# Kernel optimization log

Hardware: AMD Instinct MI355X
Metric: run time of the kernel (lower is better)

## Reference

```python
import jax, jax.numpy as jnp
import numpy as np

NUM_POINTS = 4_000_000
RADIUS = 2.5
IMG = 1024


def setup_inputs() -> dict:
    key = jax.random.key(0)
    k1, k2, k3, k4 = jax.random.split(key, 4)
    # Uniform sampling inside a sphere, mirroring the torch __init__
    phi = jax.random.uniform(k1, (NUM_POINTS,)) * 2 * np.pi
    costheta = jax.random.uniform(k2, (NUM_POINTS,)) * 2 - 1
    u = jax.random.uniform(k3, (NUM_POINTS,))
    theta = jnp.arccos(costheta)
    r = RADIUS * u ** (1.0 / 3.0)
    x = r * jnp.sin(theta) * jnp.cos(phi)
    y = r * jnp.sin(theta) * jnp.sin(phi)
    z = r * jnp.cos(theta)
    positions = jnp.stack([x, y, z], axis=-1).astype(jnp.float32)  # [N,3]
    colors = jax.random.uniform(k4, (NUM_POINTS, 3), dtype=jnp.float32)
    # Camera at origin looking down +z, points translated to z in [2.5, 7.5]
    camera_pose = jnp.eye(4, dtype=jnp.float32).at[2, 3].set(5.0)
    intrinsics = jnp.array([[800.0, 0.0, 512.0],
                            [0.0, 800.0, 512.0],
                            [0.0, 0.0, 1.0]], dtype=jnp.float32)
    return {"positions": positions, "colors": colors,
            "camera_pose": camera_pose, "intrinsics": intrinsics,
            "H": IMG, "W": IMG}


def reference(positions, colors, camera_pose, intrinsics, H, W):
    # points_cam = (R @ P^T)^T + t^T
    R = camera_pose[:3, :3]
    t = camera_pose[:3, 3]
    pc = positions @ R.T + t  # [N,3]
    x, y, z = pc[:, 0], pc[:, 1], pc[:, 2]
    fx, fy = intrinsics[0, 0], intrinsics[1, 1]
    cx, cy = intrinsics[0, 2], intrinsics[1, 2]
    u = fx * x / z + cx
    v = fy * y / z + cy
    # int() truncation toward zero, matching the torch loop
    xi = u.astype(jnp.int32)
    yi = v.astype(jnp.int32)
    valid = (xi >= 0) & (xi < W) & (yi >= 0) & (yi < H)
    n = positions.shape[0]
    pix = jnp.where(valid, yi * W + xi, H * W)  # invalid -> sentinel segment
    winner = jax.ops.segment_max(jnp.arange(n, dtype=jnp.int32), pix,
                                 num_segments=H * W + 1)[: H * W]
    has = winner >= 0  # empty segments get iinfo(int32).min
    img_flat = jnp.where(has[:, None],
                         colors[jnp.clip(winner, 0, n - 1)],
                         jnp.float32(0.0))  # [H*W, 3]
    img = img_flat.reshape(H, W, 3).transpose(2, 0, 1)[None]  # [1,3,H,W]
    return jnp.clip(img, 0.0, 1.0)
```

## Files before the change

kernel.cpp:

```cpp
#include <hip/hip_runtime.h>


#define NB      1024
#define TB      512
#define NT      1024
#define PPB_MAX 4096
#define IMGW    1024
#define IMGHW   (1024 * 1024)

__host__ __device__ __forceinline__ unsigned align8u(unsigned x) {
    return (x + 7u) & ~7u;
}

__global__ void __launch_bounds__(TB)
binsort_kernel(const float* __restrict__ pos,
               const float* __restrict__ pose,
               const float* __restrict__ intr,
               unsigned* __restrict__ bins,
               unsigned* __restrict__ histG,
               int n, int ppb, int region) {
    __shared__ unsigned stash[PPB_MAX];
    __shared__ unsigned h[NT];
    __shared__ unsigned base_[NT];
    __shared__ unsigned cur[NT];
    __shared__ unsigned sc[TB];

    int tid = threadIdx.x;
    for (int t = tid; t < NT; t += TB) h[t] = 0;
    __syncthreads();

    float r00 = pose[0], r01 = pose[1], r02 = pose[2],  t0 = pose[3];
    float r10 = pose[4], r11 = pose[5], r12 = pose[6],  t1 = pose[7];
    float r20 = pose[8], r21 = pose[9], r22 = pose[10], t2 = pose[11];
    float fx = intr[0], cx = intr[2];
    float fy = intr[4], cy = intr[5];

    int start = blockIdx.x * ppb;
    int cnt = min(start + ppb, n) - start;
    if (cnt < 0) cnt = 0;

    const float4* p4 = (const float4*)(pos + (size_t)3 * (size_t)start);
    for (int j4 = tid * 4; j4 < cnt; j4 += TB * 4) {
        int g = j4 >> 2;
        float4 A = p4[3 * g + 0];
        float4 B = p4[3 * g + 1];
        float4 C = p4[3 * g + 2];
        float xs0 = A.x, ys0 = A.y, zs0 = A.z;
        float xs1 = A.w, ys1 = B.x, zs1 = B.y;
        float xs2 = B.z, ys2 = B.w, zs2 = C.x;
        float xs3 = C.y, ys3 = C.z, zs3 = C.w;

        unsigned pv[4];
        #define PROJ(K, PX, PY, PZ)                                          \
        {                                                                    \
            float x = r00 * PX + r01 * PY + r02 * PZ + t0;                   \
            float y = r10 * PX + r11 * PY + r12 * PZ + t1;                   \
            float z = r20 * PX + r21 * PY + r22 * PZ + t2;                   \
            float u = fx * x / z + cx;                                       \
            float v = fy * y / z + cy;                                       \
            int xi = (int)u;                                                 \
            int yi = (int)v;                                                 \
            unsigned p = 0xFFFFFFFFu;                                        \
            if ((j4 + K) < cnt && xi >= 0 && xi < IMGW && yi >= 0 &&         \
                yi < IMGW) {                                                 \
                p = ((unsigned)yi << 10) | (unsigned)xi;                     \
                int tt = ((yi >> 5) << 5) + (xi >> 5);                       \
                atomicAdd(&h[tt], 1u);                                       \
            }                                                                \
            pv[K] = p;                                                       \
        }
        PROJ(0, xs0, ys0, zs0)
        PROJ(1, xs1, ys1, zs1)
        PROJ(2, xs2, ys2, zs2)
        PROJ(3, xs3, ys3, zs3)
        #undef PROJ

        if (j4 + 3 < cnt) {
            *(uint4*)&stash[j4] = make_uint4(pv[0], pv[1], pv[2], pv[3]);
        } else {
            for (int k = 0; k < 4 && j4 + k < cnt; ++k) stash[j4 + k] = pv[k];
        }
    }
    __syncthreads();

    unsigned c0 = h[2 * tid];
    unsigned c1 = h[2 * tid + 1];
    unsigned v = c0 + c1;
    sc[tid] = v;
    __syncthreads();
    for (int off = 1; off < TB; off <<= 1) {
        unsigned add = (tid >= off) ? sc[tid - off] : 0u;
        __syncthreads();
        v += add;
        sc[tid] = v;
        __syncthreads();
    }
    base_[2 * tid]     = v - c0 - c1;
    base_[2 * tid + 1] = v - c1;
    __syncthreads();

    for (int t = tid; t < NT; t += TB) {
        cur[t] = base_[t];
        histG[(size_t)t * NB + blockIdx.x] = (base_[t] << 16) | h[t];
    }
    __syncthreads();

    unsigned* myRegion = bins + (size_t)blockIdx.x * (size_t)region;
    for (int j = tid; j < cnt; j += TB) {
        unsigned pv = stash[j];
        if (pv == 0xFFFFFFFFu) continue;
        unsigned xi = pv & 1023u, yi = pv >> 10;
        unsigned t  = ((yi >> 5) << 5) + (xi >> 5);
        unsigned lp = ((yi & 31u) << 5) + (xi & 31u);
        unsigned slot = atomicAdd(&cur[t], 1u);
        myRegion[slot] = (lp << 22) | (unsigned)(start + j);
    }
}

__global__ void __launch_bounds__(TB)
paint_kernel(const unsigned* __restrict__ bins,
             const unsigned* __restrict__ histG,
             const float* __restrict__ colors,
             float* __restrict__ out,
             int region) {
    __shared__ unsigned win[NT];
    int t = blockIdx.x;
    int tid = threadIdx.x;
    for (int l = tid; l < NT; l += TB) win[l] = 0;
    __syncthreads();

    for (int b = tid; b < NB; b += TB) {
        unsigned pk = histG[(size_t)t * NB + b];
        unsigned sbase = pk >> 16, cnt = pk & 0xFFFFu;
        const unsigned* seg = bins + (size_t)b * (size_t)region + sbase;
        for (unsigned k = 0; k < cnt; ++k) {
            unsigned e = seg[k];
            atomicMax(&win[e >> 22], (e & 0x3FFFFFu) + 1u);
        }
    }
    __syncthreads();

    int tx = (t & 31) << 5, ty = (t >> 5) << 5;
    for (int l = tid; l < NT; l += TB) {
        unsigned w = win[l];
        float r = 0.0f, g = 0.0f, bl = 0.0f;
        if (w) {
            unsigned wi = w - 1u;
            r  = fminf(fmaxf(colors[3 * wi + 0], 0.0f), 1.0f);
            g  = fminf(fmaxf(colors[3 * wi + 1], 0.0f), 1.0f);
            bl = fminf(fmaxf(colors[3 * wi + 2], 0.0f), 1.0f);
        }
        int x = tx + (l & 31), y = ty + (l >> 5);
        int p = y * IMGW + x;
        out[p] = r;
        out[IMGHW + p] = g;
        out[2 * IMGHW + p] = bl;
    }
}


__global__ void proj_simple(const float* __restrict__ pos,
                            const float* __restrict__ pose,
                            const float* __restrict__ intr,
                            const int* __restrict__ Hp,
                            const int* __restrict__ Wp,
                            int* __restrict__ winner, int n) {
    int i = blockIdx.x * blockDim.x + threadIdx.x;
    if (i >= n) return;
    float px = pos[3 * i], py = pos[3 * i + 1], pz = pos[3 * i + 2];
    float x = pose[0] * px + pose[1] * py + pose[2]  * pz + pose[3];
    float y = pose[4] * px + pose[5] * py + pose[6]  * pz + pose[7];
    float z = pose[8] * px + pose[9] * py + pose[10] * pz + pose[11];
    float u = intr[0] * x / z + intr[2];
    float v = intr[4] * y / z + intr[5];
    int xi = (int)u, yi = (int)v;
    int W = *Wp, H = *Hp;
    if (xi >= 0 && xi < W && yi >= 0 && yi < H) atomicMax(&winner[yi * W + xi], i);
}

__global__ void paint_simple(const int* __restrict__ winner,
                             const float* __restrict__ colors,
                             float* __restrict__ out, int HW) {
    int p = blockIdx.x * blockDim.x + threadIdx.x;
    if (p >= HW) return;
    int w = winner[p];
    float r = 0.0f, g = 0.0f, b = 0.0f;
    if (w >= 0) {
        r = fminf(fmaxf(colors[3 * w + 0], 0.0f), 1.0f);
        g = fminf(fmaxf(colors[3 * w + 1], 0.0f), 1.0f);
        b = fminf(fmaxf(colors[3 * w + 2], 0.0f), 1.0f);
    }
    out[p] = r; out[HW + p] = g; out[2 * HW + p] = b;
}

extern "C" void kernel_launch(void* const* d_in, const int* in_sizes, int n_in,
                              void* d_out, int out_size, void* d_ws, size_t ws_size,
                              hipStream_t stream) {
    const float* positions = (const float*)d_in[0];
    const float* colors    = (const float*)d_in[1];
    const float* pose      = (const float*)d_in[2];
    const float* intr      = (const float*)d_in[3];
    const int*   Hp        = (const int*)d_in[4];
    const int*   Wp        = (const int*)d_in[5];
    float* out = (float*)d_out;

    int n  = in_sizes[0] / 3;
    int HW = out_size / 3;

    int ppb = ((n + NB - 1) / NB + 3) & ~3;
    int region = (int)align8u((unsigned)ppb);
    unsigned* bins  = (unsigned*)d_ws;
    unsigned* histG = bins + (size_t)NB * (size_t)region;
    size_t needFast = ((size_t)NB * region + (size_t)NT * NB) * sizeof(unsigned);

    bool fast = (HW == IMGHW) && (n >= 4096) && (ppb <= PPB_MAX) &&
                (n <= 4000000) && (ws_size >= needFast);

    if (fast) {
        binsort_kernel<<<NB, TB, 0, stream>>>(positions, pose, intr,
                                              bins, histG, n, ppb, region);
        paint_kernel<<<NT, TB, 0, stream>>>(bins, histG, colors, out, region);
        return;
    }

    int* winner = (int*)d_ws;
    const int block = 256;
    hipMemsetAsync(winner, 0xFF, (size_t)HW * sizeof(int), stream);
    int grid = (n + block - 1) / block;
    proj_simple<<<grid, block, 0, stream>>>(positions, pose, intr, Hp, Wp,
                                            winner, n);
    int grid2 = (HW + block - 1) / block;
    paint_simple<<<grid2, block, 0, stream>>>(winner, colors, out, HW);
}
```

Measured before the change: 70.71 us.

## Halve sort blocks, use 1024-thread binsort, align bin segments to 8

Cuts the binsort grid from 1024 to 512 blocks of 1024 threads, so each block handles about twice as many points and each thread owns one tile's histogram entry. Each tile's bin segment is now padded up to a multiple of 8 entries, with the per-block region enlarged to make room. The paint kernel assigns exactly one source block per thread, so each paint block walks half as many segments, each about twice as long. The aim is to reduce the number of histogram segments paint has to scan and to align segment starts. The cost is a larger shared stash, fewer resident binsort blocks, and longer serial per-thread loops in paint.

```diff
diff --git a/kernel.cpp b/kernel.cpp
--- a/kernel.cpp
+++ b/kernel.cpp
@@ -1,10 +1,11 @@
 #include <hip/hip_runtime.h>
 
 
-#define NB      1024
-#define TB      512
+#define NB      512
+#define TBS     1024
+#define TBP     512
 #define NT      1024
-#define PPB_MAX 4096
+#define PPB_MAX 7936
 #define IMGW    1024
 #define IMGHW   (1024 * 1024)
 
@@ -12,7 +13,7 @@
     return (x + 7u) & ~7u;
 }
 
-__global__ void __launch_bounds__(TB)
+__global__ void __launch_bounds__(TBS)
 binsort_kernel(const float* __restrict__ pos,
                const float* __restrict__ pose,
                const float* __restrict__ intr,
@@ -23,10 +24,10 @@
     __shared__ unsigned h[NT];
     __shared__ unsigned base_[NT];
     __shared__ unsigned cur[NT];
-    __shared__ unsigned sc[TB];
+    __shared__ unsigned sc[TBS];
 
     int tid = threadIdx.x;
-    for (int t = tid; t < NT; t += TB) h[t] = 0;
+    h[tid] = 0;
     __syncthreads();
 
     float r00 = pose[0], r01 = pose[1], r02 = pose[2],  t0 = pose[3];
@@ -40,7 +41,7 @@
     if (cnt < 0) cnt = 0;
 
     const float4* p4 = (const float4*)(pos + (size_t)3 * (size_t)start);
-    for (int j4 = tid * 4; j4 < cnt; j4 += TB * 4) {
+    for (int j4 = tid * 4; j4 < cnt; j4 += TBS * 4) {
         int g = j4 >> 2;
         float4 A = p4[3 * g + 0];
         float4 B = p4[3 * g + 1];
@@ -83,30 +84,26 @@
     }
     __syncthreads();
 
-    unsigned c0 = h[2 * tid];
-    unsigned c1 = h[2 * tid + 1];
-    unsigned v = c0 + c1;
+    unsigned a0 = align8u(h[tid]);
+    unsigned v = a0;
     sc[tid] = v;
     __syncthreads();
-    for (int off = 1; off < TB; off <<= 1) {
+    for (int off = 1; off < TBS; off <<= 1) {
         unsigned add = (tid >= off) ? sc[tid - off] : 0u;
         __syncthreads();
         v += add;
         sc[tid] = v;
         __syncthreads();
     }
-    base_[2 * tid]     = v - c0 - c1;
-    base_[2 * tid + 1] = v - c1;
-    __syncthreads();
-
-    for (int t = tid; t < NT; t += TB) {
-        cur[t] = base_[t];
-        histG[(size_t)t * NB + blockIdx.x] = (base_[t] << 16) | h[t];
-    }
+    base_[tid] = v - a0;
+    __syncthreads();
+
+    cur[tid] = base_[tid];
+    histG[(size_t)tid * NB + blockIdx.x] = (base_[tid] << 16) | h[tid];
     __syncthreads();
 
     unsigned* myRegion = bins + (size_t)blockIdx.x * (size_t)region;
-    for (int j = tid; j < cnt; j += TB) {
+    for (int j = tid; j < cnt; j += TBS) {
         unsigned pv = stash[j];
         if (pv == 0xFFFFFFFFu) continue;
         unsigned xi = pv & 1023u, yi = pv >> 10;
@@ -117,7 +114,7 @@
     }
 }
 
-__global__ void __launch_bounds__(TB)
+__global__ void __launch_bounds__(TBP)
 paint_kernel(const unsigned* __restrict__ bins,
              const unsigned* __restrict__ histG,
              const float* __restrict__ colors,
@@ -126,13 +123,14 @@
     __shared__ unsigned win[NT];
     int t = blockIdx.x;
     int tid = threadIdx.x;
-    for (int l = tid; l < NT; l += TB) win[l] = 0;
-    __syncthreads();
-
-    for (int b = tid; b < NB; b += TB) {
-        unsigned pk = histG[(size_t)t * NB + b];
+    win[tid] = 0;
+    win[tid + TBP] = 0;
+    __syncthreads();
+
+    {
+        unsigned pk = histG[(size_t)t * NB + tid];
         unsigned sbase = pk >> 16, cnt = pk & 0xFFFFu;
-        const unsigned* seg = bins + (size_t)b * (size_t)region + sbase;
+        const unsigned* seg = bins + (size_t)tid * (size_t)region + sbase;
         for (unsigned k = 0; k < cnt; ++k) {
             unsigned e = seg[k];
             atomicMax(&win[e >> 22], (e & 0x3FFFFFu) + 1u);
@@ -141,7 +139,7 @@
     __syncthreads();
 
     int tx = (t & 31) << 5, ty = (t >> 5) << 5;
-    for (int l = tid; l < NT; l += TB) {
+    for (int l = tid; l < NT; l += TBP) {
         unsigned w = win[l];
         float r = 0.0f, g = 0.0f, bl = 0.0f;
         if (w) {
@@ -208,18 +206,18 @@
     int HW = out_size / 3;
 
     int ppb = ((n + NB - 1) / NB + 3) & ~3;
-    int region = (int)align8u((unsigned)ppb);
+    int region = (int)align8u((unsigned)ppb) + 7 * NT;
     unsigned* bins  = (unsigned*)d_ws;
     unsigned* histG = bins + (size_t)NB * (size_t)region;
     size_t needFast = ((size_t)NB * region + (size_t)NT * NB) * sizeof(unsigned);
 
-    bool fast = (HW == IMGHW) && (n >= 4096) && (ppb <= PPB_MAX) &&
-                (n <= 4000000) && (ws_size >= needFast);
+    bool fast = (HW == IMGHW) && (n >= 4096) && ((n & 3) == 0) &&
+                (ppb <= PPB_MAX) && (n <= 4000000) && (ws_size >= needFast);
 
     if (fast) {
-        binsort_kernel<<<NB, TB, 0, stream>>>(positions, pose, intr,
-                                              bins, histG, n, ppb, region);
-        paint_kernel<<<NT, TB, 0, stream>>>(bins, histG, colors, out, region);
+        binsort_kernel<<<NB, TBS, 0, stream>>>(positions, pose, intr,
+                                               bins, histG, n, ppb, region);
+        paint_kernel<<<NT, TBP, 0, stream>>>(bins, histG, colors, out, region);
         return;
     }
 
```

After: 63.42 us. 10.3% less time.

## Paint four adjacent tiles per block and transpose histogram layout

Applied to the files above, without the earlier changes.

The paint kernel now handles groups of four consecutive tiles per 1024-thread block, one thread per source bin. Each thread reads one contiguous run of bin entries covering all four tiles, and the histogram is stored bin-major so those four counts sit next to each other. The image is written in 128-pixel-wide rows for better coalescing. Binsort drops its tail bounds checks by requiring n divisible by 4. The cost is fewer blocks (256) with more shared memory each, which may lower occupancy and parallelism.

```diff
diff --git a/kernel.cpp b/kernel.cpp
--- a/kernel.cpp
+++ b/kernel.cpp
@@ -3,7 +3,10 @@
 
 #define NB      1024
 #define TB      512
+#define TBP     1024
 #define NT      1024
+#define GP      4
+#define NG      (NT / GP)
 #define PPB_MAX 4096
 #define IMGW    1024
 #define IMGHW   (1024 * 1024)
@@ -61,8 +64,7 @@
             int xi = (int)u;                                                 \
             int yi = (int)v;                                                 \
             unsigned p = 0xFFFFFFFFu;                                        \
-            if ((j4 + K) < cnt && xi >= 0 && xi < IMGW && yi >= 0 &&         \
-                yi < IMGW) {                                                 \
+            if (xi >= 0 && xi < IMGW && yi >= 0 && yi < IMGW) {              \
                 p = ((unsigned)yi << 10) | (unsigned)xi;                     \
                 int tt = ((yi >> 5) << 5) + (xi >> 5);                       \
                 atomicAdd(&h[tt], 1u);                                       \
@@ -75,11 +77,7 @@
         PROJ(3, xs3, ys3, zs3)
         #undef PROJ
 
-        if (j4 + 3 < cnt) {
-            *(uint4*)&stash[j4] = make_uint4(pv[0], pv[1], pv[2], pv[3]);
-        } else {
-            for (int k = 0; k < 4 && j4 + k < cnt; ++k) stash[j4 + k] = pv[k];
-        }
+        *(uint4*)&stash[j4] = make_uint4(pv[0], pv[1], pv[2], pv[3]);
     }
     __syncthreads();
 
@@ -101,7 +99,7 @@
 
     for (int t = tid; t < NT; t += TB) {
         cur[t] = base_[t];
-        histG[(size_t)t * NB + blockIdx.x] = (base_[t] << 16) | h[t];
+        histG[(size_t)blockIdx.x * NT + t] = (base_[t] << 16) | h[t];
     }
     __syncthreads();
 
@@ -117,43 +115,52 @@
     }
 }
 
-__global__ void __launch_bounds__(TB)
+__global__ void __launch_bounds__(TBP)
 paint_kernel(const unsigned* __restrict__ bins,
              const unsigned* __restrict__ histG,
              const float* __restrict__ colors,
              float* __restrict__ out,
              int region) {
-    __shared__ unsigned win[NT];
-    int t = blockIdx.x;
+    __shared__ unsigned win[GP * 1024];
+    int g = blockIdx.x;
     int tid = threadIdx.x;
-    for (int l = tid; l < NT; l += TB) win[l] = 0;
-    __syncthreads();
-
-    for (int b = tid; b < NB; b += TB) {
-        unsigned pk = histG[(size_t)t * NB + b];
-        unsigned sbase = pk >> 16, cnt = pk & 0xFFFFu;
-        const unsigned* seg = bins + (size_t)b * (size_t)region + sbase;
-        for (unsigned k = 0; k < cnt; ++k) {
-            unsigned e = seg[k];
-            atomicMax(&win[e >> 22], (e & 0x3FFFFFu) + 1u);
+    #pragma unroll
+    for (int l = tid; l < GP * 1024; l += TBP) win[l] = 0;
+    __syncthreads();
+
+    {
+        const unsigned* hg = histG + (size_t)tid * NT + g * GP;
+        unsigned pk0 = hg[0], pk1 = hg[1], pk2 = hg[2], pk3 = hg[3];
+        unsigned c[GP] = {pk0 & 0xFFFFu, pk1 & 0xFFFFu,
+                          pk2 & 0xFFFFu, pk3 & 0xFFFFu};
+        const unsigned* p = bins + (size_t)tid * (size_t)region + (pk0 >> 16);
+        #pragma unroll
+        for (int s = 0; s < GP; ++s) {
+            for (unsigned k = 0; k < c[s]; ++k) {
+                unsigned e = *p++;
+                atomicMax(&win[(s << 10) + (e >> 22)],
+                          (e & 0x3FFFFFu) + 1u);
+            }
         }
     }
     __syncthreads();
 
-    int tx = (t & 31) << 5, ty = (t >> 5) << 5;
-    for (int l = tid; l < NT; l += TB) {
-        unsigned w = win[l];
-        float r = 0.0f, g = 0.0f, bl = 0.0f;
+    int tx0 = ((g * GP) & 31) << 5;
+    int ty0 = ((g * GP) >> 5) << 5;
+    for (int l = tid; l < GP * 1024; l += TBP) {
+        int lx = l & 127, ly = l >> 7;
+        int s = lx >> 5, col = lx & 31;
+        unsigned w = win[(s << 10) + (ly << 5) + col];
+        float r = 0.0f, gc = 0.0f, bl = 0.0f;
         if (w) {
             unsigned wi = w - 1u;
             r  = fminf(fmaxf(colors[3 * wi + 0], 0.0f), 1.0f);
-            g  = fminf(fmaxf(colors[3 * wi + 1], 0.0f), 1.0f);
+            gc = fminf(fmaxf(colors[3 * wi + 1], 0.0f), 1.0f);
             bl = fminf(fmaxf(colors[3 * wi + 2], 0.0f), 1.0f);
         }
-        int x = tx + (l & 31), y = ty + (l >> 5);
-        int p = y * IMGW + x;
+        int p = (ty0 + ly) * IMGW + tx0 + lx;
         out[p] = r;
-        out[IMGHW + p] = g;
+        out[IMGHW + p] = gc;
         out[2 * IMGHW + p] = bl;
     }
 }
@@ -211,15 +218,15 @@
     int region = (int)align8u((unsigned)ppb);
     unsigned* bins  = (unsigned*)d_ws;
     unsigned* histG = bins + (size_t)NB * (size_t)region;
-    size_t needFast = ((size_t)NB * region + (size_t)NT * NB) * sizeof(unsigned);
-
-    bool fast = (HW == IMGHW) && (n >= 4096) && (ppb <= PPB_MAX) &&
-                (n <= 4000000) && (ws_size >= needFast);
+    size_t needFast = ((size_t)NB * region + (size_t)NB * NT) * sizeof(unsigned);
+
+    bool fast = (HW == IMGHW) && (n >= 4096) && ((n & 3) == 0) &&
+                (ppb <= PPB_MAX) && (n <= 4000000) && (ws_size >= needFast);
 
     if (fast) {
         binsort_kernel<<<NB, TB, 0, stream>>>(positions, pose, intr,
                                               bins, histG, n, ppb, region);
-        paint_kernel<<<NT, TB, 0, stream>>>(bins, histG, colors, out, region);
+        paint_kernel<<<NG, TBP, 0, stream>>>(bins, histG, colors, out, region);
         return;
     }
 
```

Result: no change. 71.34 us (+0.9%).
